# Optimization experiments

Hardware: AMD Instinct MI355X
Metric: run time of the kernel (lower is better)

The kernel has to match this reference:

```python
import jax, jax.numpy as jnp
import numpy as np

B, S, E = 8, 1024, 512      # batch, seq, emb_size
L, H, K, F = 2, 4, 4, 128    # blocks, heads, conv kernel, final_size
I = 2 * E                    # inner dim (proj_factor=2)
DH = I // H                  # head dim
EPS = 1e-5


def _layernorm(x, g, b):
    mu = jnp.mean(x, axis=-1, keepdims=True)
    var = jnp.var(x, axis=-1, keepdims=True)
    return (x - mu) * jax.lax.rsqrt(var + EPS) * g + b


def _causal_conv(x, w, b):
    # x: [B,S,I], w: [K,I] depthwise, left-padded causal conv
    y = jax.lax.conv_general_dilated(
        x, w[:, None, :], window_strides=(1,), padding=[(K - 1, 0)],
        dimension_numbers=('NWC', 'WIO', 'NWC'), feature_group_count=I)
    return y + b


def _mlstm_parallel(q, k, v, ipre, fpre):
    # q,k,v: [B,H,S,DH]; ipre,fpre: [B,H,S]  (stabilized parallel mLSTM)
    lf = jax.nn.log_sigmoid(fpre)                       # [B,H,S]
    lfc = jnp.cumsum(lf, axis=-1)
    logD = lfc[..., :, None] - lfc[..., None, :] + ipre[..., None, :]  # [B,H,S,S]
    mask = jnp.tril(jnp.ones((S, S), dtype=bool))
    logD = jnp.where(mask, logD, -jnp.inf)
    m = jnp.max(logD, axis=-1, keepdims=True)           # [B,H,S,1]
    Dm = jnp.exp(logD - m)
    scores = jnp.einsum('bhtd,bhsd->bhts', q, k) * (DH ** -0.5) * Dm
    n = jnp.maximum(jnp.abs(jnp.sum(scores, axis=-1, keepdims=True)), jnp.exp(-m))
    return jnp.einsum('bhts,bhsd->bhtd', scores, v) / n


def _block(x, ln_g, ln_b, w_up, conv_w, conv_b, wq, wk, wv,
           w_i, b_i, w_f, b_f, skip, gn_g, w_down, b_down):
    res = x
    xn = _layernorm(x, ln_g, ln_b)
    up = xn @ w_up                                      # [B,S,2I]
    x_m, z = up[..., :I], up[..., I:]
    c_act = jax.nn.silu(_causal_conv(x_m, conv_w, conv_b))
    q = c_act @ wq
    k = c_act @ wk
    v = x_m @ wv
    qkv = jnp.concatenate([q, k, v], axis=-1)           # [B,S,3I]
    ipre = jnp.transpose(qkv @ w_i + b_i, (0, 2, 1))    # [B,H,S]
    fpre = jnp.transpose(qkv @ w_f + b_f, (0, 2, 1))
    to_h = lambda t: jnp.transpose(t.reshape(B, S, H, DH), (0, 2, 1, 3))
    h = _mlstm_parallel(to_h(q), to_h(k), to_h(v), ipre, fpre)  # [B,H,S,DH]
    # per-head group norm
    mu = jnp.mean(h, axis=-1, keepdims=True)
    var = jnp.var(h, axis=-1, keepdims=True)
    h = (h - mu) * jax.lax.rsqrt(var + EPS)
    h = jnp.transpose(h, (0, 2, 1, 3)).reshape(B, S, I) * gn_g
    h = h + skip * c_act
    h = h * jax.nn.silu(z)
    return res + h @ w_down + b_down


def setup_inputs() -> dict:
    key = jax.random.key(0)
    ks = jax.random.split(key, 12)
    n = lambda k, shp, s=0.02: jax.random.normal(k, shp, jnp.float32) * s
    return {
        'x': jax.random.normal(ks[0], (B, S, E), jnp.float32),
        'ln_g': jnp.ones((L, E), jnp.float32), 'ln_b': jnp.zeros((L, E), jnp.float32),
        'w_up': n(ks[1], (L, E, 2 * I)),
        'conv_w': n(ks[2], (L, K, I), 0.1), 'conv_b': jnp.zeros((L, I), jnp.float32),
        'wq': n(ks[3], (L, I, I)), 'wk': n(ks[4], (L, I, I)), 'wv': n(ks[5], (L, I, I)),
        'w_i': n(ks[6], (L, 3 * I, H)), 'b_i': jnp.zeros((L, H), jnp.float32),
        'w_f': n(ks[7], (L, 3 * I, H)), 'b_f': 3.0 * jnp.ones((L, H), jnp.float32),
        'skip': jnp.ones((L, I), jnp.float32), 'gn_g': jnp.ones((L, I), jnp.float32),
        'w_down': n(ks[8], (L, I, E)), 'b_down': jnp.zeros((L, E), jnp.float32),
        'w_fin': n(ks[9], (E, F)), 'b_fin': jnp.zeros((F,), jnp.float32),
    }


def reference(x, ln_g, ln_b, w_up, conv_w, conv_b, wq, wk, wv, w_i, b_i,
              w_f, b_f, skip, gn_g, w_down, b_down, w_fin, b_fin):
    h = x
    for l in range(L):  # 2 structurally identical mLSTM blocks
        h = _block(h, ln_g[l], ln_b[l], w_up[l], conv_w[l], conv_b[l],
                   wq[l], wk[l], wv[l], w_i[l], b_i[l], w_f[l], b_f[l],
                   skip[l], gn_g[l], w_down[l], b_down[l])
    return h @ w_fin + b_fin
```

## Files before the change

### kernel.cpp

```cpp
#include <hip/hip_runtime.h>
#include <math.h>

#define S_LEN 1024
#define I_DIM 1024
#define DH_   256
#define H_NUM 4
#define B_NUM 8
#define ROWS  (B_NUM*S_LEN)

#define GLOBAL_AS __attribute__((address_space(1)))
#define LDS_AS    __attribute__((address_space(3)))

#define VM0    asm volatile("s_waitcnt vmcnt(0)" ::: "memory")
#define LGKM0  asm volatile("s_waitcnt lgkmcnt(0)" ::: "memory")
#define BAR    __builtin_amdgcn_s_barrier()
#define SFENCE __builtin_amdgcn_sched_barrier(0)

typedef __attribute__((ext_vector_type(8))) short bf16x8;
typedef __attribute__((ext_vector_type(4))) float f32x4;
typedef unsigned short u16;

__device__ __forceinline__ u16 f2bf(float f) {
    union { float f; unsigned u; } v; v.f = f;
    unsigned r = v.u + 0x7FFF + ((v.u >> 16) & 1);
    return (u16)(r >> 16);
}
__device__ __forceinline__ float bf2f(u16 h) {
    union { unsigned u; float f; } v; v.u = ((unsigned)h) << 16;
    return v.f;
}

__global__ __launch_bounds__(64) void ln_fused_k(const float* __restrict__ x,
                                                 const float* __restrict__ g,
                                                 const float* __restrict__ b,
                                                 u16* __restrict__ out) {
    int row = blockIdx.x, lane = threadIdx.x;
    const float* xr = x + (size_t)row * 512;
    float4 a = *(const float4*)&xr[lane * 8];
    float4 c = *(const float4*)&xr[lane * 8 + 4];
    float s  = a.x + a.y + a.z + a.w + c.x + c.y + c.z + c.w;
    float s2 = a.x*a.x + a.y*a.y + a.z*a.z + a.w*a.w
             + c.x*c.x + c.y*c.y + c.z*c.z + c.w*c.w;
#pragma unroll
    for (int off = 32; off > 0; off >>= 1) {
        s  += __shfl_down(s, off);
        s2 += __shfl_down(s2, off);
    }
    s = __shfl(s, 0); s2 = __shfl(s2, 0);
    float mu = s * (1.f / 512.f);
    float rstd = rsqrtf(s2 * (1.f / 512.f) - mu * mu + 1e-5f);
    int e0 = lane * 8;
    float y[8] = {a.x,a.y,a.z,a.w,c.x,c.y,c.z,c.w};
    ushort4 o0, o1;
    o0.x = f2bf((y[0]-mu)*rstd*g[e0+0]+b[e0+0]);
    o0.y = f2bf((y[1]-mu)*rstd*g[e0+1]+b[e0+1]);
    o0.z = f2bf((y[2]-mu)*rstd*g[e0+2]+b[e0+2]);
    o0.w = f2bf((y[3]-mu)*rstd*g[e0+3]+b[e0+3]);
    o1.x = f2bf((y[4]-mu)*rstd*g[e0+4]+b[e0+4]);
    o1.y = f2bf((y[5]-mu)*rstd*g[e0+5]+b[e0+5]);
    o1.z = f2bf((y[6]-mu)*rstd*g[e0+6]+b[e0+6]);
    o1.w = f2bf((y[7]-mu)*rstd*g[e0+7]+b[e0+7]);
    *(ushort4*)&out[(size_t)row * 512 + e0]     = o0;
    *(ushort4*)&out[(size_t)row * 512 + e0 + 4] = o1;
}

__global__ __launch_bounds__(256) void cvtT_k(const float* __restrict__ W,
                                              u16* __restrict__ Wt, int K, int N) {
    __shared__ float t[32][33];
    int k0 = blockIdx.x * 32, n0 = blockIdx.y * 32;
    int c = threadIdx.x & 31, r8 = threadIdx.x >> 5;
#pragma unroll
    for (int q = 0; q < 4; q++) {
        int r = r8 * 4 + q;
        t[r][c] = W[(size_t)(k0 + r) * N + n0 + c];
    }
    __syncthreads();
#pragma unroll
    for (int q = 0; q < 4; q++) {
        int r = r8 * 4 + q;
        Wt[(size_t)(n0 + r) * K + k0 + c] = f2bf(t[c][r]);
    }
}

__global__ __launch_bounds__(256) void vt_k(const u16* __restrict__ v,
                                            u16* __restrict__ vt) {
    __shared__ u16 t[32][34];
    int s0 = blockIdx.x * 32, d0 = blockIdx.y * 32, bh = blockIdx.z;
    int b = bh >> 2, h = bh & 3;
    int c = threadIdx.x & 31, r4 = threadIdx.x >> 5;
#pragma unroll
    for (int q = 0; q < 4; q++) {
        int r = r4 * 4 + q;
        t[r][c] = v[(size_t)(b * 1024 + s0 + r) * I_DIM + h * 256 + d0 + c];
    }
    __syncthreads();
#pragma unroll
    for (int q = 0; q < 4; q++) {
        int r = r4 * 4 + q;
        vt[((size_t)bh * 256 + d0 + r) * 1024 + s0 + c] = t[c][r];
    }
}

template<int EPI>
__global__ __launch_bounds__(256) void gemm_bf16_k(
    const u16* __restrict__ A, const u16* __restrict__ Wt, int N, int K,
    float* __restrict__ Cf, u16* __restrict__ Cb,
    const float* __restrict__ bias, const float* __restrict__ res, int ldres)
{
    __shared__ __align__(16) u16 As[2][128 * 32];
    __shared__ __align__(16) u16 Bs[2][128 * 32];
    int tid = threadIdx.x;
    int lane = tid & 63;
    int wm = (tid >> 6) & 1, wn = tid >> 7;
    int gx = gridDim.x;
    int nwg = gx * gridDim.y;
    int bid = blockIdx.y * gx + blockIdx.x;
    int cpx = nwg >> 3;
    int swz = (bid & 7) * cpx + (bid >> 3);
    int r0 = (swz / gx) * 128, n0 = (swz % gx) * 128;

    int arow = tid >> 2, acol = (tid & 3) * 8;
    const u16* ap0 = A  + (size_t)(r0 + arow) * K + acol;
    const u16* ap1 = A  + (size_t)(r0 + 64 + arow) * K + acol;
    const u16* bp0 = Wt + (size_t)(n0 + arow) * K + acol;
    const u16* bp1 = Wt + (size_t)(n0 + 64 + arow) * K + acol;

    auto stage = [&](int kt, int bs) {
        int koff = kt * 32;
        __builtin_amdgcn_global_load_lds((const GLOBAL_AS unsigned int*)(ap0 + koff), (LDS_AS unsigned int*)&As[bs][tid * 8], 16, 0, 0);
        __builtin_amdgcn_global_load_lds((const GLOBAL_AS unsigned int*)(ap1 + koff), (LDS_AS unsigned int*)&As[bs][2048 + tid * 8], 16, 0, 0);
        __builtin_amdgcn_global_load_lds((const GLOBAL_AS unsigned int*)(bp0 + koff), (LDS_AS unsigned int*)&Bs[bs][tid * 8], 16, 0, 0);
        __builtin_amdgcn_global_load_lds((const GLOBAL_AS unsigned int*)(bp1 + koff), (LDS_AS unsigned int*)&Bs[bs][2048 + tid * 8], 16, 0, 0);
    };

    f32x4 acc[4][4];
#pragma unroll
    for (int i = 0; i < 4; i++)
#pragma unroll
        for (int j = 0; j < 4; j++) acc[i][j] = (f32x4){0.f, 0.f, 0.f, 0.f};

    int lm = lane & 15, lk = (lane >> 4) * 8;
    int nt = K >> 5;
    stage(0, 0);
    VM0; BAR; SFENCE;
    for (int t = 0; t < nt; ++t) {
        int cur = t & 1;
        if (t + 1 < nt) stage(t + 1, cur ^ 1);
        bf16x8 af[4], bfr[4];
#pragma unroll
        for (int f = 0; f < 4; f++) {
            af[f]  = *(const bf16x8*)&As[cur][(wm * 64 + f * 16 + lm) * 32 + lk];
            bfr[f] = *(const bf16x8*)&Bs[cur][(wn * 64 + f * 16 + lm) * 32 + lk];
        }
#pragma unroll
        for (int i = 0; i < 4; i++)
#pragma unroll
            for (int j = 0; j < 4; j++)
                acc[i][j] = __builtin_amdgcn_mfma_f32_16x16x32_bf16(af[i], bfr[j], acc[i][j], 0, 0, 0);
        VM0; BAR; SFENCE;
    }
    int lr = (lane >> 4) * 4;
#pragma unroll
    for (int i = 0; i < 4; i++) {
#pragma unroll
        for (int j = 0; j < 4; j++) {
#pragma unroll
            for (int q = 0; q < 4; q++) {
                int row = r0 + wm * 64 + i * 16 + lr + q;
                int col = n0 + wn * 64 + j * 16 + lm;
                float o = acc[i][j][q];
                if (EPI == 0) {
                    Cb[(size_t)row * N + col] = f2bf(o);
                } else if (EPI == 1) {
                    if (col < 1024) Cb[(size_t)row * 1024 + col] = f2bf(o);
                    else            Cf[(size_t)row * 1024 + (col - 1024)] = o;
                } else if (EPI == 2) {
                    o += bias[col] + res[(size_t)row * ldres + col];
                    Cf[(size_t)row * N + col] = o;
                    Cb[(size_t)row * N + col] = f2bf(o);
                } else {
                    o += bias[col];
                    Cf[(size_t)row * N + col] = o;
                }
            }
        }
    }
}

__global__ __launch_bounds__(256) void conv_k(const u16* __restrict__ xm,
                                              const float* __restrict__ w,
                                              const float* __restrict__ cb,
                                              u16* __restrict__ cact) {
    int idx = blockIdx.x * 256 + threadIdx.x;
    int r = idx >> 8;
    int c = (idx & 255) * 4;
    int t = r & 1023;
    const u16* base = xm + (size_t)(r - t) * I_DIM;
    float4 acc = *(const float4*)&cb[c];
#pragma unroll
    for (int j = 0; j < 4; j++) {
        int tt = t - 3 + j;
        if (tt >= 0) {
            short4 s = *(const short4*)&base[(size_t)tt * I_DIM + c];
            float4 wv = *(const float4*)&w[j * I_DIM + c];
            acc.x = fmaf(bf2f((u16)s.x), wv.x, acc.x);
            acc.y = fmaf(bf2f((u16)s.y), wv.y, acc.y);
            acc.z = fmaf(bf2f((u16)s.z), wv.z, acc.z);
            acc.w = fmaf(bf2f((u16)s.w), wv.w, acc.w);
        }
    }
    acc.x = acc.x / (1.f + __expf(-acc.x));
    acc.y = acc.y / (1.f + __expf(-acc.y));
    acc.z = acc.z / (1.f + __expf(-acc.z));
    acc.w = acc.w / (1.f + __expf(-acc.w));
    ushort4 o;
    o.x = f2bf(acc.x); o.y = f2bf(acc.y); o.z = f2bf(acc.z); o.w = f2bf(acc.w);
    *(ushort4*)&cact[(size_t)r * I_DIM + c] = o;
}

__global__ __launch_bounds__(256) void gates_k(const u16* __restrict__ q,
                                               const u16* __restrict__ k,
                                               const u16* __restrict__ v,
                                               const float* __restrict__ wi,
                                               const float* __restrict__ bi,
                                               const float* __restrict__ wf,
                                               const float* __restrict__ bf,
                                               float* __restrict__ ipre,
                                               float* __restrict__ fpre) {
    int r0 = blockIdx.x * 4;
    int tid = threadIdx.x;
    float ai[4][4], af4[4][4];
#pragma unroll
    for (int r = 0; r < 4; r++)
#pragma unroll
        for (int m = 0; m < 4; m++) { ai[r][m] = 0.f; af4[r][m] = 0.f; }
#pragma unroll
    for (int part = 0; part < 3; part++) {
        const u16* src = (part == 0 ? q : (part == 1 ? k : v)) + (size_t)r0 * I_DIM;
        const float* wip = wi + part * I_DIM * 4;
        const float* wfp = wf + part * I_DIM * 4;
#pragma unroll
        for (int jj = 0; jj < 4; jj++) {
            int e = tid + jj * 256;
            float4 w4  = *(const float4*)&wip[e * 4];
            float4 f4v = *(const float4*)&wfp[e * 4];
#pragma unroll
            for (int r = 0; r < 4; r++) {
                float xv = bf2f(src[(size_t)r * I_DIM + e]);
                ai[r][0] = fmaf(xv, w4.x, ai[r][0]);
                ai[r][1] = fmaf(xv, w4.y, ai[r][1]);
                ai[r][2] = fmaf(xv, w4.z, ai[r][2]);
                ai[r][3] = fmaf(xv, w4.w, ai[r][3]);
                af4[r][0] = fmaf(xv, f4v.x, af4[r][0]);
                af4[r][1] = fmaf(xv, f4v.y, af4[r][1]);
                af4[r][2] = fmaf(xv, f4v.z, af4[r][2]);
                af4[r][3] = fmaf(xv, f4v.w, af4[r][3]);
            }
        }
    }
#pragma unroll
    for (int off = 32; off > 0; off >>= 1) {
#pragma unroll
        for (int r = 0; r < 4; r++)
#pragma unroll
            for (int m = 0; m < 4; m++) {
                ai[r][m]  += __shfl_down(ai[r][m], off);
                af4[r][m] += __shfl_down(af4[r][m], off);
            }
    }
    __shared__ float red[4][32];
    int wv_ = tid >> 6, lane = tid & 63;
    if (lane == 0) {
#pragma unroll
        for (int r = 0; r < 4; r++)
#pragma unroll
            for (int m = 0; m < 4; m++) {
                red[wv_][r * 8 + m]     = ai[r][m];
                red[wv_][r * 8 + 4 + m] = af4[r][m];
            }
    }
    __syncthreads();
    if (tid < 32) {
        int r = tid >> 3, m = tid & 7;
        float s_ = red[0][tid] + red[1][tid] + red[2][tid] + red[3][tid];
        int row = r0 + r, bb = row >> 10, ss = row & 1023;
        if (m < 4) ipre[((size_t)(bb * 4 + m)) * 1024 + ss] = s_ + bi[m];
        else       fpre[((size_t)(bb * 4 + (m - 4))) * 1024 + ss] = s_ + bf[m - 4];
    }
}

__global__ __launch_bounds__(1024) void scan_k(const float* __restrict__ ipre,
                                               const float* __restrict__ fpre,
                                               float* __restrict__ cA,
                                               float* __restrict__ MA,
                                               float* __restrict__ nF) {
    __shared__ float buf[1024];
    int bh = blockIdx.x, t = threadIdx.x;
    size_t base = (size_t)bh * 1024;
    float fp = fpre[base + t];
    float lf = (fp >= 0.f) ? -log1pf(expf(-fp)) : (fp - log1pf(expf(fp)));
    buf[t] = lf; __syncthreads();
    for (int off = 1; off < 1024; off <<= 1) {
        float u = (t >= off) ? buf[t - off] : 0.f;
        __syncthreads();
        buf[t] += u;
        __syncthreads();
    }
    float lfc = buf[t];
    float c = ipre[base + t] - lfc;
    __syncthreads();
    buf[t] = c; __syncthreads();
    for (int off = 1; off < 1024; off <<= 1) {
        float u = (t >= off) ? buf[t - off] : -3.4e38f;
        __syncthreads();
        buf[t] = fmaxf(buf[t], u);
        __syncthreads();
    }
    float M = buf[t];
    cA[base + t] = c * 1.44269504f;
    MA[base + t] = M * 1.44269504f;
    nF[base + t] = expf(-(lfc + M));
}

__global__ __launch_bounds__(256) void attn_k(
    const u16* __restrict__ qg, const u16* __restrict__ kg, const u16* __restrict__ vt,
    const float* __restrict__ c2A, const float* __restrict__ M2A, const float* __restrict__ nFl,
    const u16* __restrict__ cact, const float* __restrict__ zb, u16* __restrict__ hb,
    const float* __restrict__ gng, const float* __restrict__ skip)
{
    __shared__ __align__(16) u16 Kb[2][32 * 256];
    __shared__ __align__(16) u16 Vb[2][256 * 32];
    __shared__ __align__(16) u16 Ps[64 * 40];
    __shared__ float rsI[64];
    __shared__ float gS[64 * 4];
    __shared__ float gQ[64 * 4];
    __shared__ float gmu[64], gvr[64];

    int tid = threadIdx.x;
    int w = tid >> 6, l = tid & 63;
    int lm = l & 15, lk = l >> 4;
    int b = blockIdx.z, h = blockIdx.y;
    int T0 = blockIdx.x * 64;
    int bh32 = b * H_NUM + h;
    size_t bh = (size_t)bh32 * S_LEN;

    bf16x8 qf[8];
    {
        size_t base = ((size_t)(b * S_LEN + T0 + w * 16 + lm)) * I_DIM + h * DH_ + lk * 8;
#pragma unroll
        for (int ks = 0; ks < 8; ks++) qf[ks] = *(const bf16x8*)&qg[base + ks * 32];
    }
    f32x4 acc[4][4];
#pragma unroll
    for (int i = 0; i < 4; i++)
#pragma unroll
        for (int jd = 0; jd < 4; jd++) acc[i][jd] = (f32x4){0.f, 0.f, 0.f, 0.f};
    float rsum[2][4] = {{0,0,0,0},{0,0,0,0}};
    float m2r[4]; int tg[4];
#pragma unroll
    for (int q = 0; q < 4; q++) {
        tg[q] = T0 + w * 16 + lk * 4 + q;
        m2r[q] = M2A[bh + tg[q]];
    }

    const size_t krow0 = ((size_t)(b * S_LEN)) * I_DIM + h * DH_;
    const size_t vrow0 = (size_t)bh32 * 256 * S_LEN;

    auto stage = [&](int s0, int bs) {
#pragma unroll
        for (int r = 0; r < 4; r++) {
            int q = r * 256 + tid;
            int row = q >> 5, cl = q & 31;
            int cs = cl ^ (row & 7);
            const u16* src = kg + krow0 + (size_t)(s0 + row) * I_DIM + cs * 8;
            __builtin_amdgcn_global_load_lds((const GLOBAL_AS unsigned int*)src,
                                             (LDS_AS unsigned int*)&Kb[bs][q * 8], 16, 0, 0);
        }
#pragma unroll
        for (int r = 0; r < 4; r++) {
            int q = r * 256 + tid;
            int dpair = q >> 3, cp = q & 7;
            int u = cp ^ (dpair & 7);
            int d = dpair * 2 + (u >> 2), c = u & 3;
            const u16* src = vt + vrow0 + (size_t)d * S_LEN + s0 + c * 8;
            __builtin_amdgcn_global_load_lds((const GLOBAL_AS unsigned int*)src,
                                             (LDS_AS unsigned int*)&Vb[bs][q * 8], 16, 0, 0);
        }
    };

    int nst = (T0 >> 5) + 2;
    stage(0, 0);
    VM0; BAR; SFENCE;
    for (int st = 0; st < nst; st++) {
        int s0 = st * 32;
        int cur = st & 1;
        if (st + 1 < nst) stage(s0 + 32, cur ^ 1);
        f32x4 sacc[2];
        sacc[0] = (f32x4){0.f,0.f,0.f,0.f};
        sacc[1] = (f32x4){0.f,0.f,0.f,0.f};
        __builtin_amdgcn_s_setprio(1);
#pragma unroll
        for (int ks = 0; ks < 8; ks++) {
#pragma unroll
            for (int js = 0; js < 2; js++) {
                int row = js * 16 + lm;
                int ch = (ks * 4 + lk) ^ (row & 7);
                bf16x8 kf = *(const bf16x8*)&Kb[cur][row * 256 + ch * 8];
                sacc[js] = __builtin_amdgcn_mfma_f32_16x16x32_bf16(qf[ks], kf, sacc[js], 0, 0, 0);
            }
        }
        __builtin_amdgcn_s_setprio(0);
#pragma unroll
        for (int js = 0; js < 2; js++) {
            int sg = s0 + js * 16 + lm;
            float c2 = c2A[bh + sg];
#pragma unroll
            for (int q = 0; q < 4; q++) {
                float v = sacc[js][q] * 0.0625f * exp2f(c2 - m2r[q]);
                v = (sg <= tg[q]) ? v : 0.f;
                u16 pb = f2bf(v);
                rsum[js][q] += bf2f(pb);
                Ps[(w * 16 + lk * 4 + q) * 40 + js * 16 + lm] = pb;
            }
        }
        LGKM0; BAR; SFENCE;
        bf16x8 vf[4];
#pragma unroll
        for (int jd = 0; jd < 4; jd++) {
            int d = w * 64 + jd * 16 + lm;
            int cp = (((d & 1) << 2) + lk) ^ ((d >> 1) & 7);
            vf[jd] = *(const bf16x8*)&Vb[cur][((d >> 1) * 8 + cp) * 8];
        }
        __builtin_amdgcn_s_setprio(1);
#pragma unroll
        for (int i = 0; i < 4; i++) {
            bf16x8 pa = *(const bf16x8*)&Ps[(i * 16 + lm) * 40 + lk * 8];
#pragma unroll
            for (int jd = 0; jd < 4; jd++)
                acc[i][jd] = __builtin_amdgcn_mfma_f32_16x16x32_bf16(pa, vf[jd], acc[i][jd], 0, 0, 0);
        }
        __builtin_amdgcn_s_setprio(0);
        VM0; BAR; SFENCE;
    }
    {
        float rq[4];
#pragma unroll
        for (int q = 0; q < 4; q++) rq[q] = rsum[0][q] + rsum[1][q];
#pragma unroll
        for (int m = 1; m < 16; m <<= 1) {
#pragma unroll
            for (int q = 0; q < 4; q++) rq[q] += __shfl_xor(rq[q], m);
        }
        if (lm == 0) {
#pragma unroll
            for (int q = 0; q < 4; q++) rsI[w * 16 + lk * 4 + q] = rq[q];
        }
    }
    __syncthreads();
    if (tid < 64) {
        float n = fmaxf(fabsf(rsI[tid]), nFl[bh + T0 + tid]);
        rsI[tid] = 1.f / n;
    }
    __syncthreads();
#pragma unroll
    for (int i = 0; i < 4; i++) {
#pragma unroll
        for (int q = 0; q < 4; q++) {
            int rl = i * 16 + lk * 4 + q;
            float inv = rsI[rl];
            float ps = 0.f, pq = 0.f;
#pragma unroll
            for (int jd = 0; jd < 4; jd++) {
                float v = acc[i][jd][q] * inv;
                acc[i][jd][q] = v;
                ps += v; pq += v * v;
            }
#pragma unroll
            for (int m = 1; m < 16; m <<= 1) {
                ps += __shfl_xor(ps, m);
                pq += __shfl_xor(pq, m);
            }
            if (lm == 0) { gS[rl * 4 + w] = ps; gQ[rl * 4 + w] = pq; }
        }
    }
    __syncthreads();
    if (tid < 64) {
        float s1 = gS[tid*4] + gS[tid*4+1] + gS[tid*4+2] + gS[tid*4+3];
        float s2 = gQ[tid*4] + gQ[tid*4+1] + gQ[tid*4+2] + gQ[tid*4+3];
        float mu = s1 * (1.f / 256.f);
        float var = s2 * (1.f / 256.f) - mu * mu;
        gmu[tid] = mu;
        gvr[tid] = rsqrtf(var + 1e-5f);
    }
    __syncthreads();
#pragma unroll
    for (int i = 0; i < 4; i++) {
#pragma unroll
        for (int q = 0; q < 4; q++) {
            int rl = i * 16 + lk * 4 + q;
            size_t r = (size_t)b * S_LEN + T0 + rl;
            float mu = gmu[rl], rv = gvr[rl];
#pragma unroll
            for (int jd = 0; jd < 4; jd++) {
                int cix = h * DH_ + w * 64 + jd * 16 + lm;
                float val = (acc[i][jd][q] - mu) * rv * gng[cix];
                float ca = bf2f(cact[r * I_DIM + cix]);
                float z = zb[r * I_DIM + cix];
                float hm = (val + skip[cix] * ca) * (z / (1.f + __expf(-z)));
                hb[r * I_DIM + cix] = f2bf(hm);
            }
        }
    }
}

extern "C" void kernel_launch(void* const* d_in, const int* in_sizes, int n_in,
                              void* d_out, int out_size, void* d_ws, size_t ws_size,
                              hipStream_t stream) {
    const float* x      = (const float*)d_in[0];
    const float* ln_g   = (const float*)d_in[1];
    const float* ln_b   = (const float*)d_in[2];
    const float* w_up   = (const float*)d_in[3];
    const float* conv_w = (const float*)d_in[4];
    const float* conv_b = (const float*)d_in[5];
    const float* wq     = (const float*)d_in[6];
    const float* wk     = (const float*)d_in[7];
    const float* wv     = (const float*)d_in[8];
    const float* w_i    = (const float*)d_in[9];
    const float* b_i    = (const float*)d_in[10];
    const float* w_f    = (const float*)d_in[11];
    const float* b_f    = (const float*)d_in[12];
    const float* skip   = (const float*)d_in[13];
    const float* gn_g   = (const float*)d_in[14];
    const float* w_down = (const float*)d_in[15];
    const float* b_down = (const float*)d_in[16];
    const float* w_fin  = (const float*)d_in[17];
    const float* b_fin  = (const float*)d_in[18];

    char* p = (char*)d_ws;
    auto alloc = [&](size_t bytes) { void* r = p; p += (bytes + 255) & ~(size_t)255; return r; };
    float* zbuf  = (float*)alloc((size_t)ROWS * 1024 * 4);
    float* xa    = (float*)alloc((size_t)ROWS * 512 * 4);
    float* xb2   = (float*)alloc((size_t)ROWS * 512 * 4);
    u16*  xln    = (u16*)alloc((size_t)ROWS * 512 * 2);
    u16*  xm     = (u16*)alloc((size_t)ROWS * 1024 * 2);
    u16*  cactb  = (u16*)alloc((size_t)ROWS * 1024 * 2);
    u16*  qbf    = (u16*)alloc((size_t)ROWS * 1024 * 2);
    u16*  kbf    = (u16*)alloc((size_t)ROWS * 1024 * 2);
    u16*  vbf    = (u16*)alloc((size_t)ROWS * 1024 * 2);
    u16*  vtg    = (u16*)alloc((size_t)32 * 256 * 1024 * 2);
    u16*  hbf    = (u16*)alloc((size_t)ROWS * 1024 * 2);
    u16*  xoutb  = (u16*)alloc((size_t)ROWS * 512 * 2);
    u16*  wupT   = (u16*)alloc((size_t)2 * 2048 * 512 * 2);
    u16*  wqT    = (u16*)alloc((size_t)2 * 1024 * 1024 * 2);
    u16*  wkT    = (u16*)alloc((size_t)2 * 1024 * 1024 * 2);
    u16*  wvT    = (u16*)alloc((size_t)2 * 1024 * 1024 * 2);
    u16*  wdT    = (u16*)alloc((size_t)2 * 512 * 1024 * 2);
    u16*  wfT    = (u16*)alloc((size_t)128 * 512 * 2);
    float* ipre  = (float*)alloc(32768 * 4);
    float* fpre  = (float*)alloc(32768 * 4);
    float* cA    = (float*)alloc(32768 * 4);
    float* MA    = (float*)alloc(32768 * 4);
    float* nF    = (float*)alloc(32768 * 4);

    for (int l = 0; l < 2; l++) {
        cvtT_k<<<dim3(16, 64), 256, 0, stream>>>(w_up + (size_t)l * 512 * 2048, wupT + (size_t)l * 2048 * 512, 512, 2048);
        cvtT_k<<<dim3(32, 32), 256, 0, stream>>>(wq + (size_t)l * 1024 * 1024, wqT + (size_t)l * 1024 * 1024, 1024, 1024);
        cvtT_k<<<dim3(32, 32), 256, 0, stream>>>(wk + (size_t)l * 1024 * 1024, wkT + (size_t)l * 1024 * 1024, 1024, 1024);
        cvtT_k<<<dim3(32, 32), 256, 0, stream>>>(wv + (size_t)l * 1024 * 1024, wvT + (size_t)l * 1024 * 1024, 1024, 1024);
        cvtT_k<<<dim3(32, 16), 256, 0, stream>>>(w_down + (size_t)l * 1024 * 512, wdT + (size_t)l * 512 * 1024, 1024, 512);
    }
    cvtT_k<<<dim3(16, 4), 256, 0, stream>>>(w_fin, wfT, 512, 128);

    const float* xin = x;
    for (int l = 0; l < 2; l++) {
        float* xout = (l == 0) ? xa : xb2;
        ln_fused_k<<<ROWS, 64, 0, stream>>>(xin, ln_g + l * 512, ln_b + l * 512, xln);
        gemm_bf16_k<1><<<dim3(16, 64), 256, 0, stream>>>(
            xln, wupT + (size_t)l * 2048 * 512, 2048, 512, zbuf, xm, nullptr, nullptr, 0);
        conv_k<<<ROWS, 256, 0, stream>>>(xm, conv_w + l * 4 * I_DIM, conv_b + l * I_DIM, cactb);
        gemm_bf16_k<0><<<dim3(8, 64), 256, 0, stream>>>(
            xm, wvT + (size_t)l * 1024 * 1024, 1024, 1024, nullptr, vbf, nullptr, nullptr, 0);
        gemm_bf16_k<0><<<dim3(8, 64), 256, 0, stream>>>(
            cactb, wqT + (size_t)l * 1024 * 1024, 1024, 1024, nullptr, qbf, nullptr, nullptr, 0);
        gemm_bf16_k<0><<<dim3(8, 64), 256, 0, stream>>>(
            cactb, wkT + (size_t)l * 1024 * 1024, 1024, 1024, nullptr, kbf, nullptr, nullptr, 0);
        vt_k<<<dim3(32, 8, 32), 256, 0, stream>>>(vbf, vtg);
        gates_k<<<ROWS / 4, 256, 0, stream>>>(qbf, kbf, vbf,
            w_i + l * 3072 * 4, b_i + l * 4, w_f + l * 3072 * 4, b_f + l * 4, ipre, fpre);
        scan_k<<<32, 1024, 0, stream>>>(ipre, fpre, cA, MA, nF);
        attn_k<<<dim3(16, 4, 8), 256, 0, stream>>>(qbf, kbf, vtg, cA, MA, nF, cactb, zbuf, hbf,
            gn_g + l * I_DIM, skip + l * I_DIM);
        gemm_bf16_k<2><<<dim3(4, 64), 256, 0, stream>>>(
            hbf, wdT + (size_t)l * 512 * 1024, 512, 1024, xout, xoutb,
            b_down + l * 512, xin, 512);
        xin = xout;
    }
    gemm_bf16_k<3><<<dim3(1, 64), 256, 0, stream>>>(
        xoutb, wfT, 128, 512, (float*)d_out, nullptr, b_fin, nullptr, 0);
}
```

Baseline: 696.5 us.

## Load V fragments directly into registers, prefetch c2, reverse tile order

Drops the LDS staging buffer for V in the attention kernel. Each wave now loads its V MFMA fragments straight from global memory into double-buffered registers, and the c2 gate values are prefetched one stage ahead as well. The block index is reversed so the longest causal tiles launch first, improving load balance across CUs. This removes LDS traffic and LDS usage for V, at the cost of more VGPR pressure and uncoalesced per-lane global loads that may not be hidden.

After: 693.9 us. Within noise of the previous version (-0.4%).

```diff
diff --git a/kernel.cpp b/kernel.cpp
--- a/kernel.cpp
+++ b/kernel.cpp
@@ -329,7 +329,6 @@
     const float* __restrict__ gng, const float* __restrict__ skip)
 {
     __shared__ __align__(16) u16 Kb[2][32 * 256];
-    __shared__ __align__(16) u16 Vb[2][256 * 32];
     __shared__ __align__(16) u16 Ps[64 * 40];
     __shared__ float rsI[64];
     __shared__ float gS[64 * 4];
@@ -340,7 +339,7 @@
     int w = tid >> 6, l = tid & 63;
     int lm = l & 15, lk = l >> 4;
     int b = blockIdx.z, h = blockIdx.y;
-    int T0 = blockIdx.x * 64;
+    int T0 = (15 - blockIdx.x) * 64;
     int bh32 = b * H_NUM + h;
     size_t bh = (size_t)bh32 * S_LEN;
 
@@ -364,9 +363,9 @@
     }
 
     const size_t krow0 = ((size_t)(b * S_LEN)) * I_DIM + h * DH_;
-    const size_t vrow0 = (size_t)bh32 * 256 * S_LEN;
-
-    auto stage = [&](int s0, int bs) {
+    const u16* vptr = vt + (size_t)bh32 * 256 * S_LEN + (size_t)(w * 64 + lm) * S_LEN + lk * 8;
+
+    auto stageK = [&](int s0, int bs) {
 #pragma unroll
         for (int r = 0; r < 4; r++) {
             int q = r * 256 + tid;
@@ -376,25 +375,29 @@
             __builtin_amdgcn_global_load_lds((const GLOBAL_AS unsigned int*)src,
                                              (LDS_AS unsigned int*)&Kb[bs][q * 8], 16, 0, 0);
         }
-#pragma unroll
-        for (int r = 0; r < 4; r++) {
-            int q = r * 256 + tid;
-            int dpair = q >> 3, cp = q & 7;
-            int u = cp ^ (dpair & 7);
-            int d = dpair * 2 + (u >> 2), c = u & 3;
-            const u16* src = vt + vrow0 + (size_t)d * S_LEN + s0 + c * 8;
-            __builtin_amdgcn_global_load_lds((const GLOBAL_AS unsigned int*)src,
-                                             (LDS_AS unsigned int*)&Vb[bs][q * 8], 16, 0, 0);
-        }
     };
 
     int nst = (T0 >> 5) + 2;
-    stage(0, 0);
+    stageK(0, 0);
+    bf16x8 vA[4], vB[4];
+    float c2c[2], c2n[2];
+#pragma unroll
+    for (int jd = 0; jd < 4; jd++) vA[jd] = *(const bf16x8*)(vptr + jd * 16 * S_LEN);
+    c2c[0] = c2A[bh + lm];
+    c2c[1] = c2A[bh + 16 + lm];
     VM0; BAR; SFENCE;
+
     for (int st = 0; st < nst; st++) {
         int s0 = st * 32;
         int cur = st & 1;
-        if (st + 1 < nst) stage(s0 + 32, cur ^ 1);
+        int more = (st + 1 < nst);
+        if (more) {
+            stageK(s0 + 32, cur ^ 1);
+#pragma unroll
+            for (int jd = 0; jd < 4; jd++) vB[jd] = *(const bf16x8*)(vptr + jd * 16 * S_LEN + s0 + 32);
+            c2n[0] = c2A[bh + s0 + 32 + lm];
+            c2n[1] = c2A[bh + s0 + 48 + lm];
+        }
         f32x4 sacc[2];
         sacc[0] = (f32x4){0.f,0.f,0.f,0.f};
         sacc[1] = (f32x4){0.f,0.f,0.f,0.f};
@@ -413,10 +416,9 @@
 #pragma unroll
         for (int js = 0; js < 2; js++) {
             int sg = s0 + js * 16 + lm;
-            float c2 = c2A[bh + sg];
 #pragma unroll
             for (int q = 0; q < 4; q++) {
-                float v = sacc[js][q] * 0.0625f * exp2f(c2 - m2r[q]);
+                float v = sacc[js][q] * 0.0625f * __builtin_amdgcn_exp2f(c2c[js] - m2r[q]);
                 v = (sg <= tg[q]) ? v : 0.f;
                 u16 pb = f2bf(v);
                 rsum[js][q] += bf2f(pb);
@@ -424,23 +426,21 @@
             }
         }
         LGKM0; BAR; SFENCE;
-        bf16x8 vf[4];
-#pragma unroll
-        for (int jd = 0; jd < 4; jd++) {
-            int d = w * 64 + jd * 16 + lm;
-            int cp = (((d & 1) << 2) + lk) ^ ((d >> 1) & 7);
-            vf[jd] = *(const bf16x8*)&Vb[cur][((d >> 1) * 8 + cp) * 8];
-        }
         __builtin_amdgcn_s_setprio(1);
 #pragma unroll
         for (int i = 0; i < 4; i++) {
             bf16x8 pa = *(const bf16x8*)&Ps[(i * 16 + lm) * 40 + lk * 8];
 #pragma unroll
             for (int jd = 0; jd < 4; jd++)
-                acc[i][jd] = __builtin_amdgcn_mfma_f32_16x16x32_bf16(pa, vf[jd], acc[i][jd], 0, 0, 0);
+                acc[i][jd] = __builtin_amdgcn_mfma_f32_16x16x32_bf16(pa, vA[jd], acc[i][jd], 0, 0, 0);
         }
         __builtin_amdgcn_s_setprio(0);
         VM0; BAR; SFENCE;
+        if (more) {
+#pragma unroll
+            for (int jd = 0; jd < 4; jd++) vA[jd] = vB[jd];
+            c2c[0] = c2n[0]; c2c[1] = c2n[1];
+        }
     }
     {
         float rq[4];
```
